# Kernel tuning notes

Measured on AMD Instinct MI355X. Metric: run time of the kernel, lower is better.

## Reference

```python
import jax, jax.numpy as jnp
import numpy as np

V, N = 3, 32768
C2, C3 = 256, 32          # feat_ch_2D, feat_ch_3D
H = W = 128               # 2D feature map size
D = 32                    # 3D volume feature size
CIN = C2 + C3             # 288, MLP in_channels


def setup_inputs() -> dict:
    key = jax.random.key(0)
    ks = jax.random.split(key, 16)
    sc = 0.02
    inp = {
        'pts': jax.random.uniform(ks[0], (1, N, 3), minval=-0.5, maxval=0.5),
        'pts_proj': jax.random.uniform(ks[1], (1, N, 2), minval=-1.0, maxval=1.0),
        'img_feat0': jax.random.normal(ks[2], (V, C2, H, W)),
        'img_feat1': jax.random.normal(ks[3], (V, C2, H, W)),
        'vol_feat0': jax.random.normal(ks[4], (V, C3, D, D, D)),
        'vol_feat1': jax.random.normal(ks[5], (V, C3, D, D, D)),
        'W0': jax.random.normal(ks[6], (1024, CIN)) * sc,  'b0': jnp.zeros((1024,)),
        'W1': jax.random.normal(ks[7], (512, CIN + 1024)) * sc, 'b1': jnp.zeros((512,)),
        'W2': jax.random.normal(ks[8], (256, CIN + 512)) * sc,  'b2': jnp.zeros((256,)),
        'W3': jax.random.normal(ks[9], (128, CIN + 256)) * sc,  'b3': jnp.zeros((128,)),
        'W4': jax.random.normal(ks[10], (1, 128)) * sc,         'b4': jnp.zeros((1,)),
        'mean_num': 3,
    }
    return inp


def _gs2d(feat, gx, gy):
    # feat: [C,H,W]; gx,gy: [N] normalized coords in [-1,1]
    C, Hh, Ww = feat.shape
    ix = jnp.clip(((gx + 1.0) * Ww - 1.0) * 0.5, 0.0, Ww - 1.0)  # align_corners=False, border pad
    iy = jnp.clip(((gy + 1.0) * Hh - 1.0) * 0.5, 0.0, Hh - 1.0)
    x0f, y0f = jnp.floor(ix), jnp.floor(iy)
    wx, wy = ix - x0f, iy - y0f
    x0 = x0f.astype(jnp.int32); x1 = jnp.minimum(x0 + 1, Ww - 1)
    y0 = y0f.astype(jnp.int32); y1 = jnp.minimum(y0 + 1, Hh - 1)
    v00 = feat[:, y0, x0]; v01 = feat[:, y0, x1]
    v10 = feat[:, y1, x0]; v11 = feat[:, y1, x1]
    return (v00 * (1 - wy) * (1 - wx) + v01 * (1 - wy) * wx
            + v10 * wy * (1 - wx) + v11 * wy * wx)  # [C,N]


def _gs3d(feat, gx, gy, gz):
    # feat: [C,D,H,W]; grid x->W, y->H, z->D (torch grid_sample convention)
    C, Dd, Hh, Ww = feat.shape
    ix = jnp.clip(((gx + 1.0) * Ww - 1.0) * 0.5, 0.0, Ww - 1.0)
    iy = jnp.clip(((gy + 1.0) * Hh - 1.0) * 0.5, 0.0, Hh - 1.0)
    iz = jnp.clip(((gz + 1.0) * Dd - 1.0) * 0.5, 0.0, Dd - 1.0)
    x0f, y0f, z0f = jnp.floor(ix), jnp.floor(iy), jnp.floor(iz)
    wx, wy, wz = ix - x0f, iy - y0f, iz - z0f
    x0 = x0f.astype(jnp.int32); x1 = jnp.minimum(x0 + 1, Ww - 1)
    y0 = y0f.astype(jnp.int32); y1 = jnp.minimum(y0 + 1, Hh - 1)
    z0 = z0f.astype(jnp.int32); z1 = jnp.minimum(z0 + 1, Dd - 1)
    def g(zi, yi, xi):
        return feat[:, zi, yi, xi]  # [C,N]
    out = (g(z0, y0, x0) * (1 - wz) * (1 - wy) * (1 - wx)
           + g(z0, y0, x1) * (1 - wz) * (1 - wy) * wx
           + g(z0, y1, x0) * (1 - wz) * wy * (1 - wx)
           + g(z0, y1, x1) * (1 - wz) * wy * wx
           + g(z1, y0, x0) * wz * (1 - wy) * (1 - wx)
           + g(z1, y0, x1) * wz * (1 - wy) * wx
           + g(z1, y1, x0) * wz * wy * (1 - wx)
           + g(z1, y1, x1) * wz * wy * wx)
    return out  # [C,N]


def _lrelu(x):
    return jnp.where(x >= 0, x, 0.2 * x)


def _conv1x1(Wm, bm, x):
    # x: [V,C,N] -> [V,O,N]
    return jnp.einsum('oc,vcn->von', Wm, x) + bm[None, :, None]


def _mlp0(x, W0, b0, W1, b1, W2, b2, W3, b3):
    out = _lrelu(_conv1x1(W0, b0, x))
    out = _lrelu(_conv1x1(W1, b1, jnp.concatenate([x, out], axis=1)))
    out = _lrelu(_conv1x1(W2, b2, jnp.concatenate([x, out], axis=1)))
    out = _lrelu(_conv1x1(W3, b3, jnp.concatenate([x, out], axis=1)))
    return out  # [V,128,N]


def _forward(pts, pts_proj, img_feats, vol_feats,
             W0, b0, W1, b1, W2, b2, W3, b3, W4, b4, mean_num):
    v = img_feats[0].shape[0]
    gx2 = jnp.broadcast_to(pts_proj[:, :, 0], (v, pts_proj.shape[1]))
    gy2 = jnp.broadcast_to(pts_proj[:, :, 1], (v, pts_proj.shape[1]))
    p = pts * 2.0  # pts *= 2.0 before 3D sampling
    gx3 = jnp.broadcast_to(p[:, :, 0], (v, p.shape[1]))
    gy3 = jnp.broadcast_to(p[:, :, 1], (v, p.shape[1]))
    gz3 = jnp.broadcast_to(p[:, :, 2], (v, p.shape[1]))
    outs = []
    for img_feat, vol_feat in zip(img_feats, vol_feats):
        f2 = jax.vmap(_gs2d)(img_feat, gx2, gy2)            # [V,C2,N]
        f3 = jax.vmap(_gs3d)(vol_feat, gx3, gy3, gz3)       # [V,C3,N]
        pt_feat = jnp.concatenate([f2, f3], axis=1)         # [V,288,N]
        pt_out0 = _mlp0(pt_feat, W0, b0, W1, b1, W2, b2, W3, b3)
        pt_out0_mean = jnp.mean(pt_out0[:mean_num], axis=0, keepdims=True)  # [1,128,N]
        sdf = jax.nn.sigmoid(_conv1x1(W4, b4, pt_out0_mean))                # [1,1,N]
        outs.append(jnp.transpose(sdf, (0, 2, 1)))                          # [1,N,1]
    return tuple(outs)


def reference(pts, pts_proj, img_feat0, img_feat1, vol_feat0, vol_feat1,
              W0, b0, W1, b1, W2, b2, W3, b3, W4, b4, mean_num):
    return _forward(pts, pts_proj, [img_feat0, img_feat1], [vol_feat0, vol_feat1],
                    W0, b0, W1, b1, W2, b2, W3, b3, W4, b4, mean_num)
```

## Files before the change

kernel.cpp:

```cpp
#include <hip/hip_runtime.h>
#include <hip/hip_bf16.h>

#define NV 3
#define NPTS 32768
#define C2C 256
#define C3C 32
#define CINC 288
#define CINP 320
#define HH 128
#define WWW 128
#define DDD 32

typedef short bh8 __attribute__((ext_vector_type(8)));
typedef float fx4 __attribute__((ext_vector_type(4)));
typedef unsigned short us4 __attribute__((ext_vector_type(4)));

__device__ __forceinline__ float b2f(unsigned short u) {
    unsigned int x = ((unsigned int)u) << 16;
    return __uint_as_float(x);
}
__device__ __forceinline__ unsigned short f2b(float f) {
    unsigned int x = __float_as_uint(f);
    unsigned int r = (x + 0x7FFFu + ((x >> 16) & 1u)) >> 16;
    return (unsigned short)r;
}

__device__ __forceinline__ void gl2lds16(const unsigned short* g, unsigned short* l) {
    __builtin_amdgcn_global_load_lds(
        (const __attribute__((address_space(1))) unsigned int*)g,
        (__attribute__((address_space(3))) unsigned int*)l, 16, 0, 0);
}

__device__ __forceinline__ int xcd_swz(int orig, int nwg) {
    int xcd = orig & 7;
    int q = nwg >> 3, r = nwg & 7;
    int base = (xcd < r) ? xcd * (q + 1) : r * (q + 1) + (xcd - r) * q;
    return base + (orig >> 3);
}

__global__ void k_wpad4(const float* __restrict__ s0, const float* __restrict__ s1,
                        const float* __restrict__ s2, const float* __restrict__ s3,
                        unsigned short* __restrict__ d0, unsigned short* __restrict__ d1,
                        unsigned short* __restrict__ d2, unsigned short* __restrict__ d3) {
    const int Ms[4] = {1024, 512, 256, 128};
    const int Kps[4] = {320, 1344, 832, 576};
    int i = blockIdx.y;
    int M = Ms[i], Kp = Kps[i];
    int idx = blockIdx.x * 256 + threadIdx.x;
    if (idx >= M * Kp) return;
    const float* src = (i == 0) ? s0 : (i == 1) ? s1 : (i == 2) ? s2 : s3;
    unsigned short* dst = (i == 0) ? d0 : (i == 1) ? d1 : (i == 2) ? d2 : d3;
    int m = idx / Kp, k = idx - m * Kp;
    int Ksrc = Kp - 32;
    float v;
    if (k < CINC) v = src[(size_t)m * Ksrc + k];
    else if (k < CINP) v = 0.0f;
    else v = src[(size_t)m * Ksrc + (k - 32)];
    dst[idx] = f2b(v);
}

__global__ void k_timg(const float* __restrict__ in0, const float* __restrict__ in1,
                       unsigned short* __restrict__ out, size_t lvlStride) {
    int lvl = blockIdx.z >> 2, cb = blockIdx.z & 3;
    const float* in = lvl ? in1 : in0;
    int v = blockIdx.x >> 7, y = blockIdx.x & 127;
    int x0 = blockIdx.y << 6, c0 = cb << 6;
    __shared__ float t[64][65];
    int tx = threadIdx.x & 63, tg = threadIdx.x >> 6;
    const float* src = in + (((size_t)(v * C2C + c0) * HH + y) * WWW + x0);
#pragma unroll
    for (int i = 0; i < 16; i++) {
        int cl = tg * 16 + i;
        t[cl][tx] = src[(size_t)cl * (HH * WWW) + tx];
    }
    __syncthreads();
    unsigned short* dst = out + lvl * lvlStride + ((size_t)(v * HH + y) * WWW + x0) * C2C + c0;
#pragma unroll
    for (int i = 0; i < 16; i++) {
        int xl = tg * 16 + i;
        dst[(size_t)xl * C2C + tx] = f2b(t[tx][xl]);
    }
}

__global__ void k_tvol(const float* __restrict__ in0, const float* __restrict__ in1,
                       unsigned short* __restrict__ out, size_t lvlStride) {
    int lvl = blockIdx.z;
    const float* in = lvl ? in1 : in0;
    int v = blockIdx.x;
    int s0 = blockIdx.y << 8;
    __shared__ float t[32][257];
    int tid = threadIdx.x;
    const float* src = in + (size_t)v * C3C * 32768 + s0;
#pragma unroll
    for (int c = 0; c < 32; c++) t[c][tid] = src[(size_t)c * 32768 + tid];
    __syncthreads();
    unsigned short* dst = out + lvl * lvlStride + ((size_t)v * 32768 + s0) * C3C;
    int c = tid & 31, sb = tid >> 5;
#pragma unroll
    for (int j = 0; j < 32; j++) {
        int sl = j * 8 + sb;
        dst[(size_t)sl * C3C + c] = f2b(t[c][sl]);
    }
}

__device__ __forceinline__ void sample_body(const float* __restrict__ pts, const float* __restrict__ proj,
                         const unsigned short* __restrict__ imgT, const unsigned short* __restrict__ volT,
                         unsigned short* __restrict__ ptT, int n0, int Nk) {
    int w = threadIdx.x >> 6, l = threadIdx.x & 63;
    int i = blockIdx.x * 4 + w;
    int v = blockIdx.y;
    int n = n0 + i;
    unsigned short* dstRow = ptT + (size_t)(v * Nk + i) * CINP;

    {
        float gx = proj[n * 2 + 0], gy = proj[n * 2 + 1];
        float ix = fminf(fmaxf(((gx + 1.0f) * (float)WWW - 1.0f) * 0.5f, 0.0f), (float)(WWW - 1));
        float iy = fminf(fmaxf(((gy + 1.0f) * (float)HH - 1.0f) * 0.5f, 0.0f), (float)(HH - 1));
        float x0f = floorf(ix), y0f = floorf(iy);
        float wx = ix - x0f, wy = iy - y0f;
        int x0 = (int)x0f, y0 = (int)y0f;
        int x1 = min(x0 + 1, WWW - 1), y1 = min(y0 + 1, HH - 1);
        const unsigned short* base = imgT + (size_t)v * HH * WWW * C2C;
        us4 a = *((const us4*)(base + ((size_t)(y0 * WWW + x0)) * C2C) + l);
        us4 b = *((const us4*)(base + ((size_t)(y0 * WWW + x1)) * C2C) + l);
        us4 c = *((const us4*)(base + ((size_t)(y1 * WWW + x0)) * C2C) + l);
        us4 d = *((const us4*)(base + ((size_t)(y1 * WWW + x1)) * C2C) + l);
        float w00 = (1.0f - wy) * (1.0f - wx), w01 = (1.0f - wy) * wx;
        float w10 = wy * (1.0f - wx), w11 = wy * wx;
        us4 rv;
#pragma unroll
        for (int r = 0; r < 4; r++) {
            float f = b2f(a[r]) * w00 + b2f(b[r]) * w01 + b2f(c[r]) * w10 + b2f(d[r]) * w11;
            rv[r] = f2b(f);
        }
        *(us4*)(dstRow + l * 4) = rv;
    }
    {
        float gx = pts[n * 3 + 0] * 2.0f, gy = pts[n * 3 + 1] * 2.0f, gz = pts[n * 3 + 2] * 2.0f;
        float ix = fminf(fmaxf(((gx + 1.0f) * (float)DDD - 1.0f) * 0.5f, 0.0f), (float)(DDD - 1));
        float iy = fminf(fmaxf(((gy + 1.0f) * (float)DDD - 1.0f) * 0.5f, 0.0f), (float)(DDD - 1));
        float iz = fminf(fmaxf(((gz + 1.0f) * (float)DDD - 1.0f) * 0.5f, 0.0f), (float)(DDD - 1));
        float x0f = floorf(ix), y0f = floorf(iy), z0f = floorf(iz);
        float wx = ix - x0f, wy = iy - y0f, wz = iz - z0f;
        int x0 = (int)x0f, y0 = (int)y0f, z0 = (int)z0f;
        int x1 = min(x0 + 1, DDD - 1), y1 = min(y0 + 1, DDD - 1), z1 = min(z0 + 1, DDD - 1);
        int c = l & 31, zs = l >> 5;
        int zi = zs ? z1 : z0;
        float wzs = zs ? wz : (1.0f - wz);
        const unsigned short* base = volT + (size_t)v * 32768 * C3C;
        float f00 = b2f(base[((size_t)((zi * 32 + y0) * 32 + x0)) * C3C + c]);
        float f01 = b2f(base[((size_t)((zi * 32 + y0) * 32 + x1)) * C3C + c]);
        float f10 = b2f(base[((size_t)((zi * 32 + y1) * 32 + x0)) * C3C + c]);
        float f11 = b2f(base[((size_t)((zi * 32 + y1) * 32 + x1)) * C3C + c]);
        float r = (f00 * (1.0f - wy) * (1.0f - wx) + f01 * (1.0f - wy) * wx +
                   f10 * wy * (1.0f - wx) + f11 * wy * wx) * wzs;
        float other = __shfl_xor(r, 32);
        r += other;
        if (zs == 0) dstRow[C2C + c] = f2b(r);
    }
    if (l < 8) *(us4*)(dstRow + CINC + l * 4) = (us4){0, 0, 0, 0};
}

__global__ __launch_bounds__(256) void k_sampleL0(const float* p, const float* pr, const unsigned short* im,
                                                  const unsigned short* vo, unsigned short* pt, int n0, int Nk) {
    sample_body(p, pr, im, vo, pt, n0, Nk);
}
__global__ __launch_bounds__(256) void k_sampleL1(const float* p, const float* pr, const unsigned short* im,
                                                  const unsigned short* vo, unsigned short* pt, int n0, int Nk) {
    sample_body(p, pr, im, vo, pt, n0, Nk);
}

template <int K2, int M>
__device__ __forceinline__ void gemm128_body(const unsigned short* __restrict__ A,
                                             const unsigned short* __restrict__ B1,
                                             const unsigned short* __restrict__ B2,
                                             const float* __restrict__ bias,
                                             unsigned short* __restrict__ C) {
    constexpr int K1 = CINP;
    constexpr int K = K1 + K2;
    constexpr int nt1 = K1 / 32;
    constexpr int nt = K / 32;
    __shared__ unsigned short Ash[3][128 * 32];
    __shared__ unsigned short Bsh[3][128 * 32];
    int tid = threadIdx.x;
    int w = tid >> 6, l = tid & 63;
    int la = l & 15, lg = l >> 4;
    int wm = w & 1, wn = w >> 1;
    int gx = gridDim.x;
    int nwg = gx * gridDim.y;
    int bid = xcd_swz(blockIdx.y * gx + blockIdx.x, nwg);
    int mBlk = (bid % gx) * 128;
    int nBlk = (bid / gx) * 128;
    int sRow = l >> 2, sCol = (l & 3) * 8;
    int r0 = w * 32 + sRow, r1 = r0 + 16;

    const unsigned short* Ag = A + (size_t)mBlk * K;
    const unsigned short* B1g = B1 + (size_t)nBlk * K1;
    const unsigned short* B2g = (K2 > 0) ? (B2 + (size_t)nBlk * K2) : (const unsigned short*)0;

    fx4 acc[4][4];
#pragma unroll
    for (int mi = 0; mi < 4; mi++)
#pragma unroll
        for (int ni = 0; ni < 4; ni++) acc[mi][ni] = (fx4){0.f, 0.f, 0.f, 0.f};

    auto stage = [&](int t, int b) {
        const unsigned short* as = Ag + t * 32 + sCol;
        gl2lds16(as + (size_t)r0 * K, &Ash[b][r0 * 32 + sCol]);
        gl2lds16(as + (size_t)r1 * K, &Ash[b][r1 * 32 + sCol]);
        const unsigned short* bs;
        size_t ldb;
        if (t < nt1) { bs = B1g + t * 32 + sCol; ldb = (size_t)K1; }
        else         { bs = B2g + (t - nt1) * 32 + sCol; ldb = (size_t)K2; }
        gl2lds16(bs + (size_t)r0 * ldb, &Bsh[b][r0 * 32 + sCol]);
        gl2lds16(bs + (size_t)r1 * ldb, &Bsh[b][r1 * 32 + sCol]);
    };

    stage(0, 0);
    if (nt > 1) stage(1, 1);
    asm volatile("s_waitcnt vmcnt(4)" ::: "memory");
    __builtin_amdgcn_s_barrier();
    int cur = 0, nxt2 = 2;
    for (int t = 0; t < nt; t++) {
        if (t + 2 < nt) stage(t + 2, nxt2);
        bh8 af[4], bfv[4];
#pragma unroll
        for (int mi = 0; mi < 4; mi++) af[mi] = *(const bh8*)&Ash[cur][(wm * 64 + mi * 16 + la) * 32 + lg * 8];
#pragma unroll
        for (int ni = 0; ni < 4; ni++) bfv[ni] = *(const bh8*)&Bsh[cur][(wn * 64 + ni * 16 + la) * 32 + lg * 8];
#pragma unroll
        for (int mi = 0; mi < 4; mi++)
#pragma unroll
            for (int ni = 0; ni < 4; ni++)
                acc[mi][ni] = __builtin_amdgcn_mfma_f32_16x16x32_bf16(af[mi], bfv[ni], acc[mi][ni], 0, 0, 0);
        asm volatile("s_waitcnt lgkmcnt(0)" ::: "memory");
        if (t + 2 < nt)      asm volatile("s_waitcnt vmcnt(4)" ::: "memory");
        else if (t + 1 < nt) asm volatile("s_waitcnt vmcnt(0)" ::: "memory");
        __builtin_amdgcn_s_barrier();
        cur = (cur == 2) ? 0 : cur + 1;
        nxt2 = (nxt2 == 2) ? 0 : nxt2 + 1;
    }

#pragma unroll
    for (int mi = 0; mi < 4; mi++) {
        int m0 = mBlk + wm * 64 + mi * 16 + lg * 4;
        fx4 bb = *(const fx4*)(bias + m0);
#pragma unroll
        for (int ni = 0; ni < 4; ni++) {
            int n = nBlk + wn * 64 + ni * 16 + la;
            us4 rv;
#pragma unroll
            for (int r = 0; r < 4; r++) {
                float x = acc[mi][ni][r] + bb[r];
                x = (x >= 0.0f) ? x : 0.2f * x;
                rv[r] = f2b(x);
            }
            *(us4*)(C + (size_t)n * M + m0) = rv;
        }
    }
}

__global__ __launch_bounds__(256) void k_g0L0(const unsigned short* A, const unsigned short* B1,
                                              const float* b, unsigned short* C) { gemm128_body<0, 1024>(A, B1, nullptr, b, C); }
__global__ __launch_bounds__(256) void k_g0L1(const unsigned short* A, const unsigned short* B1,
                                              const float* b, unsigned short* C) { gemm128_body<0, 1024>(A, B1, nullptr, b, C); }
__global__ __launch_bounds__(256) void k_g2L0(const unsigned short* A, const unsigned short* B1, const unsigned short* B2,
                                              const float* b, unsigned short* C) { gemm128_body<512, 256>(A, B1, B2, b, C); }
__global__ __launch_bounds__(256) void k_g2L1(const unsigned short* A, const unsigned short* B1, const unsigned short* B2,
                                              const float* b, unsigned short* C) { gemm128_body<512, 256>(A, B1, B2, b, C); }
__global__ __launch_bounds__(256) void k_g3L0(const unsigned short* A, const unsigned short* B1, const unsigned short* B2,
                                              const float* b, unsigned short* C) { gemm128_body<256, 128>(A, B1, B2, b, C); }
__global__ __launch_bounds__(256) void k_g3L1(const unsigned short* A, const unsigned short* B1, const unsigned short* B2,
                                              const float* b, unsigned short* C) { gemm128_body<256, 128>(A, B1, B2, b, C); }

__device__ __forceinline__ void g1_body(const unsigned short* __restrict__ A,
                                        const unsigned short* __restrict__ B1,
                                        const unsigned short* __restrict__ B2,
                                        const float* __restrict__ bias,
                                        unsigned short* __restrict__ C) {
    constexpr int Kp = 1344;
    constexpr int K2 = 1024;
    constexpr int M = 512;
    constexpr int nt = Kp >> 6;
    __shared__ unsigned short As[2][256 * 64];
    __shared__ unsigned short Bs[2][256 * 64];
    int tid = threadIdx.x;
    int w = tid >> 6, l = tid & 63;
    int la = l & 15, lg = l >> 4;
    int wm = w >> 2, wn = w & 3;
    int gx = gridDim.x;
    int nwg = gx * gridDim.y;
    int bid = xcd_swz(blockIdx.y * gx + blockIdx.x, nwg);
    int mBlk = (bid % gx) * 256;
    int nBlk = (bid / gx) * 256;

    const unsigned short* Ag = A + (size_t)mBlk * Kp;

    fx4 acc[8][4];
#pragma unroll
    for (int mi = 0; mi < 8; mi++)
#pragma unroll
        for (int ni = 0; ni < 4; ni++) acc[mi][ni] = (fx4){0.f, 0.f, 0.f, 0.f};

    auto stageB = [&](int t, int nxt) {
        const unsigned short* bsrc;
        size_t ldb;
        int kc;
        if (t < 5) { bsrc = B1; ldb = CINP; kc = t * 64; }
        else       { bsrc = B2; ldb = (size_t)K2; kc = (t - 5) * 64; }
        bsrc += (size_t)nBlk * ldb + kc;
#pragma unroll
        for (int h = 0; h < 2; h++)
#pragma unroll
            for (int j = 0; j < 2; j++) {
                int idx = j * 512 + tid;
                int r = (h << 7) + (idx >> 3);
                int c = (idx & 7) ^ (r & 7);
                gl2lds16(bsrc + (size_t)r * ldb + c * 8, &Bs[nxt][(h << 13) + idx * 8]);
            }
    };
    auto stageA1 = [&](int t, int nxt) {
        const unsigned short* asrc = Ag + t * 64;
#pragma unroll
        for (int h = 0; h < 2; h++) {
            int idx = tid;
            int r = (h << 7) + (idx >> 3);
            int c = (idx & 7) ^ (r & 7);
            gl2lds16(asrc + (size_t)r * Kp + c * 8, &As[nxt][(h << 13) + idx * 8]);
        }
    };
    auto stageA2 = [&](int t, int nxt) {
        const unsigned short* asrc = Ag + t * 64;
#pragma unroll
        for (int h = 0; h < 2; h++) {
            int idx = 512 + tid;
            int r = (h << 7) + (idx >> 3);
            int c = (idx & 7) ^ (r & 7);
            gl2lds16(asrc + (size_t)r * Kp + c * 8, &As[nxt][(h << 13) + idx * 8]);
        }
    };

    stageB(0, 0);
    stageA1(0, 0);
    stageA2(0, 0);
    asm volatile("s_waitcnt vmcnt(0)" ::: "memory");
    __builtin_amdgcn_s_barrier();

    for (int t = 0; t < nt; t++) {
        int cur = t & 1;
        const unsigned short* Ab = &As[cur][0];
        const unsigned short* Bb = &Bs[cur][0];
        bh8 afr[4][2];
#pragma unroll
        for (int p = 0; p < 4; p++) {
            int qm = p >> 1, qn = p & 1;
            if (qn == 0) {
#pragma unroll
                for (int m2 = 0; m2 < 4; m2++)
#pragma unroll
                    for (int s = 0; s < 2; s++) {
                        int row = wm * 128 + (qm * 4 + m2) * 16 + la;
                        int c = (s * 4 + lg) ^ (row & 7);
                        afr[m2][s] = *(const bh8*)&Ab[row * 64 + c * 8];
                    }
            }
            bh8 bfr[2][2];
#pragma unroll
            for (int n2 = 0; n2 < 2; n2++)
#pragma unroll
                for (int s = 0; s < 2; s++) {
                    int row = wn * 64 + (qn * 2 + n2) * 16 + la;
                    int c = (s * 4 + lg) ^ (row & 7);
                    bfr[n2][s] = *(const bh8*)&Bb[row * 64 + c * 8];
                }
            if (p == 0 && t + 1 < nt) stageB(t + 1, cur ^ 1);
            if (p == 1 && t + 1 < nt) stageA1(t + 1, cur ^ 1);
            if (p == 2 && t + 1 < nt) stageA2(t + 1, cur ^ 1);
            __builtin_amdgcn_s_barrier();
            __builtin_amdgcn_s_setprio(1);
#pragma unroll
            for (int m2 = 0; m2 < 4; m2++)
#pragma unroll
                for (int n2 = 0; n2 < 2; n2++)
#pragma unroll
                    for (int s = 0; s < 2; s++)
                        acc[qm * 4 + m2][qn * 2 + n2] = __builtin_amdgcn_mfma_f32_16x16x32_bf16(
                            afr[m2][s], bfr[n2][s], acc[qm * 4 + m2][qn * 2 + n2], 0, 0, 0);
            __builtin_amdgcn_s_setprio(0);
            if (p == 1) {
                if (t + 1 < nt) asm volatile("s_waitcnt vmcnt(6)" ::: "memory");
                else            asm volatile("s_waitcnt vmcnt(0)" ::: "memory");
            }
            if (p == 3) {
                asm volatile("s_waitcnt lgkmcnt(0)" ::: "memory");
                if (t + 1 < nt) asm volatile("s_waitcnt vmcnt(2)" ::: "memory");
            }
            __builtin_amdgcn_s_barrier();
        }
    }

#pragma unroll
    for (int mi = 0; mi < 8; mi++) {
        int m0 = mBlk + wm * 128 + mi * 16 + lg * 4;
        fx4 bb = *(const fx4*)(bias + m0);
#pragma unroll
        for (int ni = 0; ni < 4; ni++) {
            int n = nBlk + wn * 64 + ni * 16 + la;
            us4 rv;
#pragma unroll
            for (int r = 0; r < 4; r++) {
                float x = acc[mi][ni][r] + bb[r];
                x = (x >= 0.0f) ? x : 0.2f * x;
                rv[r] = f2b(x);
            }
            *(us4*)(C + (size_t)n * M + m0) = rv;
        }
    }
}

__global__ __launch_bounds__(512) void k_g1L0(const unsigned short* A, const unsigned short* B1, const unsigned short* B2,
                                              const float* b, unsigned short* C) { g1_body(A, B1, B2, b, C); }
__global__ __launch_bounds__(512) void k_g1L1(const unsigned short* A, const unsigned short* B1, const unsigned short* B2,
                                              const float* b, unsigned short* C) { g1_body(A, B1, B2, b, C); }

__device__ __forceinline__ void head_body(const unsigned short* __restrict__ o3, const float* __restrict__ W4,
                       const float* __restrict__ b4, const int* __restrict__ mn_p,
                       float* __restrict__ out, int n0, int Nk, int level) {
    int wv = threadIdx.x >> 6, l = threadIdx.x & 63;
    int sub = l >> 4, cl = l & 15;
    int i = blockIdx.x * 16 + wv * 4 + sub;
    if (i >= Nk) return;
    int mn = *mn_p;
    if (mn > NV) mn = NV;
    if (mn < 1) mn = 1;
    fx4 w0 = *(const fx4*)(W4 + cl * 8);
    fx4 w1 = *(const fx4*)(W4 + cl * 8 + 4);
    float s = 0.0f;
    for (int v = 0; v < mn; v++) {
        bh8 x = *(const bh8*)(o3 + (size_t)(v * Nk + i) * 128 + cl * 8);
#pragma unroll
        for (int r = 0; r < 4; r++) s += w0[r] * b2f((unsigned short)x[r]);
#pragma unroll
        for (int r = 0; r < 4; r++) s += w1[r] * b2f((unsigned short)x[4 + r]);
    }
#pragma unroll
    for (int m = 1; m < 16; m <<= 1) s += __shfl_xor(s, m);
    if (cl == 0) {
        s = s / (float)mn + b4[0];
        out[(size_t)level * NPTS + n0 + i] = 1.0f / (1.0f + expf(-s));
    }
}

__global__ __launch_bounds__(256) void k_headL0(const unsigned short* o3, const float* W4, const float* b4,
                                                const int* mn, float* out, int n0, int Nk) {
    head_body(o3, W4, b4, mn, out, n0, Nk, 0);
}
__global__ __launch_bounds__(256) void k_headL1(const unsigned short* o3, const float* W4, const float* b4,
                                                const int* mn, float* out, int n0, int Nk) {
    head_body(o3, W4, b4, mn, out, n0, Nk, 1);
}

extern "C" void kernel_launch(void* const* d_in, const int* in_sizes, int n_in,
                              void* d_out, int out_size, void* d_ws, size_t ws_size,
                              hipStream_t stream) {
    const float* pts = (const float*)d_in[0];
    const float* proj = (const float*)d_in[1];
    const float* img[2] = {(const float*)d_in[2], (const float*)d_in[3]};
    const float* vol[2] = {(const float*)d_in[4], (const float*)d_in[5]};
    const float* Wf[4] = {(const float*)d_in[6], (const float*)d_in[8], (const float*)d_in[10], (const float*)d_in[12]};
    const float* bf[4] = {(const float*)d_in[7], (const float*)d_in[9], (const float*)d_in[11], (const float*)d_in[13]};
    const float* W4 = (const float*)d_in[14];
    const float* b4 = (const float*)d_in[15];
    const int* mn = (const int*)d_in[16];
    float* out = (float*)d_out;

    const int Kp[4] = {320, 1344, 832, 576};
    const int Msz[4] = {1024, 512, 256, 128};

    char* ws = (char*)d_ws;
    size_t off = 0;
    auto alloc = [&](size_t bytes) -> char* {
        char* p = ws + off;
        off = (off + bytes + 255) & ~(size_t)255;
        return p;
    };

    const size_t imgStride = (size_t)NV * HH * WWW * C2C;
    const size_t volStride = (size_t)NV * 32768 * C3C;

    unsigned short* Wb[4];
    for (int i = 0; i < 4; i++) Wb[i] = (unsigned short*)alloc((size_t)Msz[i] * Kp[i] * 2);
    unsigned short* imgT = (unsigned short*)alloc(2 * imgStride * 2);
    unsigned short* volT = (unsigned short*)alloc(2 * volStride * 2);
    size_t fixed = off;

    const size_t perPt = (size_t)NV * 2 * (CINP + 1024 + 512);
    int Nk = NPTS;
    if (fixed + (size_t)Nk * perPt + 4096 > ws_size) {
        size_t avail = (ws_size > fixed + 4096) ? (ws_size - fixed - 4096) : 0;
        long nk = (long)(avail / perPt);
        nk = (nk / 512) * 512;
        if (nk < 512) nk = 512;
        if (nk > NPTS) nk = NPTS;
        Nk = (int)nk;
    }
    unsigned short* ptT = (unsigned short*)alloc((size_t)NV * Nk * CINP * 2);
    unsigned short* o0 = (unsigned short*)alloc((size_t)NV * Nk * 1024 * 2);
    unsigned short* o1 = (unsigned short*)alloc((size_t)NV * Nk * 512 * 2);
    unsigned short* o2 = o0;
    unsigned short* o3 = o0 + (size_t)NV * Nk * 256;

    k_wpad4<<<dim3(2688, 4), 256, 0, stream>>>(Wf[0], Wf[1], Wf[2], Wf[3], Wb[0], Wb[1], Wb[2], Wb[3]);
    k_timg<<<dim3(NV * HH, WWW / 64, 8), 256, 0, stream>>>(img[0], img[1], imgT, imgStride);
    k_tvol<<<dim3(NV, 32768 / 256, 2), 256, 0, stream>>>(vol[0], vol[1], volT, volStride);

    for (int n0 = 0; n0 < NPTS; n0 += Nk) {
        int nk = NPTS - n0 < Nk ? NPTS - n0 : Nk;
        int NC = NV * nk;
        k_sampleL0<<<dim3(nk / 4, NV), 256, 0, stream>>>(pts, proj, imgT, volT, ptT, n0, nk);
        k_g0L0<<<dim3(1024 / 128, NC / 128), 256, 0, stream>>>(Wb[0], ptT, bf[0], o0);
        k_g1L0<<<dim3(512 / 256, NC / 256), 512, 0, stream>>>(Wb[1], ptT, o0, bf[1], o1);
        k_g2L0<<<dim3(256 / 128, NC / 128), 256, 0, stream>>>(Wb[2], ptT, o1, bf[2], o2);
        k_g3L0<<<dim3(128 / 128, NC / 128), 256, 0, stream>>>(Wb[3], ptT, o2, bf[3], o3);
        k_headL0<<<(nk + 15) / 16, 256, 0, stream>>>(o3, W4, b4, mn, out, n0, nk);
        k_sampleL1<<<dim3(nk / 4, NV), 256, 0, stream>>>(pts, proj, imgT + imgStride, volT + volStride, ptT, n0, nk);
        k_g0L1<<<dim3(1024 / 128, NC / 128), 256, 0, stream>>>(Wb[0], ptT, bf[0], o0);
        k_g1L1<<<dim3(512 / 256, NC / 256), 512, 0, stream>>>(Wb[1], ptT, o0, bf[1], o1);
        k_g2L1<<<dim3(256 / 128, NC / 128), 256, 0, stream>>>(Wb[2], ptT, o1, bf[2], o2);
        k_g3L1<<<dim3(128 / 128, NC / 128), 256, 0, stream>>>(Wb[3], ptT, o2, bf[3], o3);
        k_headL1<<<(nk + 15) / 16, 256, 0, stream>>>(o3, W4, b4, mn, out, n0, nk);
    }
}
```

Before: 1.059 ms.

## Use 256x256 tile GEMM for layer 0 and merge prep kernels into one launch

The first MLP layer GEMM now runs through the 256x256, 512-thread templated kernel previously used only for layer 1, in place of the 128x128 kernel. This raises per-block data reuse and cuts the number of blocks. The three preprocessing kernels (weight padding/cast, image transpose, volume transpose) are merged into one launch that dispatches on block index, removing two launches. The risk is that layer 0 has a short K (320), so the large tile gives few pipeline iterations and fewer blocks for occupancy.

New measurement: 1.065 ms. About the same (+0.6%).

```diff
diff --git a/kernel.cpp b/kernel.cpp
--- a/kernel.cpp
+++ b/kernel.cpp
@@ -38,68 +38,74 @@
     return base + (orig >> 3);
 }
 
-__global__ void k_wpad4(const float* __restrict__ s0, const float* __restrict__ s1,
-                        const float* __restrict__ s2, const float* __restrict__ s3,
-                        unsigned short* __restrict__ d0, unsigned short* __restrict__ d1,
-                        unsigned short* __restrict__ d2, unsigned short* __restrict__ d3) {
-    const int Ms[4] = {1024, 512, 256, 128};
-    const int Kps[4] = {320, 1344, 832, 576};
-    int i = blockIdx.y;
-    int M = Ms[i], Kp = Kps[i];
-    int idx = blockIdx.x * 256 + threadIdx.x;
-    if (idx >= M * Kp) return;
-    const float* src = (i == 0) ? s0 : (i == 1) ? s1 : (i == 2) ? s2 : s3;
-    unsigned short* dst = (i == 0) ? d0 : (i == 1) ? d1 : (i == 2) ? d2 : d3;
-    int m = idx / Kp, k = idx - m * Kp;
-    int Ksrc = Kp - 32;
-    float v;
-    if (k < CINC) v = src[(size_t)m * Ksrc + k];
-    else if (k < CINP) v = 0.0f;
-    else v = src[(size_t)m * Ksrc + (k - 32)];
-    dst[idx] = f2b(v);
-}
-
-__global__ void k_timg(const float* __restrict__ in0, const float* __restrict__ in1,
-                       unsigned short* __restrict__ out, size_t lvlStride) {
-    int lvl = blockIdx.z >> 2, cb = blockIdx.z & 3;
-    const float* in = lvl ? in1 : in0;
-    int v = blockIdx.x >> 7, y = blockIdx.x & 127;
-    int x0 = blockIdx.y << 6, c0 = cb << 6;
-    __shared__ float t[64][65];
-    int tx = threadIdx.x & 63, tg = threadIdx.x >> 6;
-    const float* src = in + (((size_t)(v * C2C + c0) * HH + y) * WWW + x0);
-#pragma unroll
-    for (int i = 0; i < 16; i++) {
-        int cl = tg * 16 + i;
-        t[cl][tx] = src[(size_t)cl * (HH * WWW) + tx];
-    }
-    __syncthreads();
-    unsigned short* dst = out + lvl * lvlStride + ((size_t)(v * HH + y) * WWW + x0) * C2C + c0;
-#pragma unroll
-    for (int i = 0; i < 16; i++) {
-        int xl = tg * 16 + i;
-        dst[(size_t)xl * C2C + tx] = f2b(t[tx][xl]);
-    }
-}
-
-__global__ void k_tvol(const float* __restrict__ in0, const float* __restrict__ in1,
-                       unsigned short* __restrict__ out, size_t lvlStride) {
-    int lvl = blockIdx.z;
-    const float* in = lvl ? in1 : in0;
-    int v = blockIdx.x;
-    int s0 = blockIdx.y << 8;
-    __shared__ float t[32][257];
-    int tid = threadIdx.x;
-    const float* src = in + (size_t)v * C3C * 32768 + s0;
-#pragma unroll
-    for (int c = 0; c < 32; c++) t[c][tid] = src[(size_t)c * 32768 + tid];
-    __syncthreads();
-    unsigned short* dst = out + lvl * lvlStride + ((size_t)v * 32768 + s0) * C3C;
-    int c = tid & 31, sb = tid >> 5;
-#pragma unroll
-    for (int j = 0; j < 32; j++) {
-        int sl = j * 8 + sb;
-        dst[(size_t)sl * C3C + c] = f2b(t[c][sl]);
+__global__ __launch_bounds__(256) void k_prep(
+    const float* __restrict__ s0, const float* __restrict__ s1,
+    const float* __restrict__ s2, const float* __restrict__ s3,
+    unsigned short* __restrict__ d0, unsigned short* __restrict__ d1,
+    unsigned short* __restrict__ d2, unsigned short* __restrict__ d3,
+    const float* __restrict__ img0, const float* __restrict__ img1,
+    unsigned short* __restrict__ imgT, size_t imgStride,
+    const float* __restrict__ vol0, const float* __restrict__ vol1,
+    unsigned short* __restrict__ volT, size_t volStride) {
+    __shared__ float smem[32 * 257];
+    int b = blockIdx.x;
+    if (b < 5088) {
+        int base, M, Kp;
+        const float* src;
+        unsigned short* dst;
+        if (b < 1280)      { base = 0;    M = 1024; Kp = 320;  src = s0; dst = d0; }
+        else if (b < 3968) { base = 1280; M = 512;  Kp = 1344; src = s1; dst = d1; }
+        else if (b < 4800) { base = 3968; M = 256;  Kp = 832;  src = s2; dst = d2; }
+        else               { base = 4800; M = 128;  Kp = 576;  src = s3; dst = d3; }
+        int idx = (b - base) * 256 + threadIdx.x;
+        if (idx >= M * Kp) return;
+        int m = idx / Kp, k = idx - m * Kp;
+        int Ksrc = Kp - 32;
+        float v;
+        if (k < CINC) v = src[(size_t)m * Ksrc + k];
+        else if (k < CINP) v = 0.0f;
+        else v = src[(size_t)m * Ksrc + (k - 32)];
+        dst[idx] = f2b(v);
+    } else if (b < 11232) {
+        int id = b - 5088;
+        int bx = id % 384, by = (id / 384) & 1, bz = id / 768;
+        int lvl = bz >> 2, cb = bz & 3;
+        const float* in = lvl ? img1 : img0;
+        int v = bx >> 7, y = bx & 127;
+        int x0 = by << 6, c0 = cb << 6;
+        float (*t)[65] = (float(*)[65])smem;
+        int tx = threadIdx.x & 63, tg = threadIdx.x >> 6;
+        const float* src = in + (((size_t)(v * C2C + c0) * HH + y) * WWW + x0);
+#pragma unroll
+        for (int i = 0; i < 16; i++) {
+            int cl = tg * 16 + i;
+            t[cl][tx] = src[(size_t)cl * (HH * WWW) + tx];
+        }
+        __syncthreads();
+        unsigned short* dst = imgT + lvl * imgStride + ((size_t)(v * HH + y) * WWW + x0) * C2C + c0;
+#pragma unroll
+        for (int i = 0; i < 16; i++) {
+            int xl = tg * 16 + i;
+            dst[(size_t)xl * C2C + tx] = f2b(t[tx][xl]);
+        }
+    } else {
+        int id = b - 11232;
+        int v = id % 3, sy = (id / 3) & 127, lvl = id / 384;
+        const float* in = lvl ? vol1 : vol0;
+        int s0i = sy << 8;
+        float (*t)[257] = (float(*)[257])smem;
+        int tid = threadIdx.x;
+        const float* src = in + (size_t)v * C3C * 32768 + s0i;
+#pragma unroll
+        for (int c = 0; c < 32; c++) t[c][tid] = src[(size_t)c * 32768 + tid];
+        __syncthreads();
+        unsigned short* dst = volT + lvl * volStride + ((size_t)v * 32768 + s0i) * C3C;
+        int c = tid & 31, sb = tid >> 5;
+#pragma unroll
+        for (int j = 0; j < 32; j++) {
+            int sl = j * 8 + sb;
+            dst[(size_t)sl * C3C + c] = f2b(t[c][sl]);
+        }
     }
 }
 
@@ -260,10 +266,6 @@
     }
 }
 
-__global__ __launch_bounds__(256) void k_g0L0(const unsigned short* A, const unsigned short* B1,
-                                              const float* b, unsigned short* C) { gemm128_body<0, 1024>(A, B1, nullptr, b, C); }
-__global__ __launch_bounds__(256) void k_g0L1(const unsigned short* A, const unsigned short* B1,
-                                              const float* b, unsigned short* C) { gemm128_body<0, 1024>(A, B1, nullptr, b, C); }
 __global__ __launch_bounds__(256) void k_g2L0(const unsigned short* A, const unsigned short* B1, const unsigned short* B2,
                                               const float* b, unsigned short* C) { gemm128_body<512, 256>(A, B1, B2, b, C); }
 __global__ __launch_bounds__(256) void k_g2L1(const unsigned short* A, const unsigned short* B1, const unsigned short* B2,
@@ -273,15 +275,13 @@
 __global__ __launch_bounds__(256) void k_g3L1(const unsigned short* A, const unsigned short* B1, const unsigned short* B2,
                                               const float* b, unsigned short* C) { gemm128_body<256, 128>(A, B1, B2, b, C); }
 
-__device__ __forceinline__ void g1_body(const unsigned short* __restrict__ A,
-                                        const unsigned short* __restrict__ B1,
-                                        const unsigned short* __restrict__ B2,
-                                        const float* __restrict__ bias,
-                                        unsigned short* __restrict__ C) {
-    constexpr int Kp = 1344;
-    constexpr int K2 = 1024;
-    constexpr int M = 512;
-    constexpr int nt = Kp >> 6;
+template <int KP, int K2, int M>
+__device__ __forceinline__ void g1t_body(const unsigned short* __restrict__ A,
+                                         const unsigned short* __restrict__ B1,
+                                         const unsigned short* __restrict__ B2,
+                                         const float* __restrict__ bias,
+                                         unsigned short* __restrict__ C) {
+    constexpr int nt = KP >> 6;
     __shared__ unsigned short As[2][256 * 64];
     __shared__ unsigned short Bs[2][256 * 64];
     int tid = threadIdx.x;
@@ -294,7 +294,7 @@
     int mBlk = (bid % gx) * 256;
     int nBlk = (bid / gx) * 256;
 
-    const unsigned short* Ag = A + (size_t)mBlk * Kp;
+    const unsigned short* Ag = A + (size_t)mBlk * KP;
 
     fx4 acc[8][4];
 #pragma unroll
@@ -326,7 +326,7 @@
             int idx = tid;
             int r = (h << 7) + (idx >> 3);
             int c = (idx & 7) ^ (r & 7);
-            gl2lds16(asrc + (size_t)r * Kp + c * 8, &As[nxt][(h << 13) + idx * 8]);
+            gl2lds16(asrc + (size_t)r * KP + c * 8, &As[nxt][(h << 13) + idx * 8]);
         }
     };
     auto stageA2 = [&](int t, int nxt) {
@@ -336,7 +336,7 @@
             int idx = 512 + tid;
             int r = (h << 7) + (idx >> 3);
             int c = (idx & 7) ^ (r & 7);
-            gl2lds16(asrc + (size_t)r * Kp + c * 8, &As[nxt][(h << 13) + idx * 8]);
+            gl2lds16(asrc + (size_t)r * KP + c * 8, &As[nxt][(h << 13) + idx * 8]);
         }
     };
 
@@ -418,10 +418,14 @@
     }
 }
 
+__global__ __launch_bounds__(512) void k_g0L0(const unsigned short* A, const unsigned short* B1,
+                                              const float* b, unsigned short* C) { g1t_body<320, 0, 1024>(A, B1, nullptr, b, C); }
+__global__ __launch_bounds__(512) void k_g0L1(const unsigned short* A, const unsigned short* B1,
+                                              const float* b, unsigned short* C) { g1t_body<320, 0, 1024>(A, B1, nullptr, b, C); }
 __global__ __launch_bounds__(512) void k_g1L0(const unsigned short* A, const unsigned short* B1, const unsigned short* B2,
-                                              const float* b, unsigned short* C) { g1_body(A, B1, B2, b, C); }
+                                              const float* b, unsigned short* C) { g1t_body<1344, 1024, 512>(A, B1, B2, b, C); }
 __global__ __launch_bounds__(512) void k_g1L1(const unsigned short* A, const unsigned short* B1, const unsigned short* B2,
-                                              const float* b, unsigned short* C) { g1_body(A, B1, B2, b, C); }
+                                              const float* b, unsigned short* C) { g1t_body<1344, 1024, 512>(A, B1, B2, b, C); }
 
 __device__ __forceinline__ void head_body(const unsigned short* __restrict__ o3, const float* __restrict__ W4,
                        const float* __restrict__ b4, const int* __restrict__ mn_p,
@@ -510,21 +514,20 @@
     unsigned short* o2 = o0;
     unsigned short* o3 = o0 + (size_t)NV * Nk * 256;
 
-    k_wpad4<<<dim3(2688, 4), 256, 0, stream>>>(Wf[0], Wf[1], Wf[2], Wf[3], Wb[0], Wb[1], Wb[2], Wb[3]);
-    k_timg<<<dim3(NV * HH, WWW / 64, 8), 256, 0, stream>>>(img[0], img[1], imgT, imgStride);
-    k_tvol<<<dim3(NV, 32768 / 256, 2), 256, 0, stream>>>(vol[0], vol[1], volT, volStride);
+    k_prep<<<12000, 256, 0, stream>>>(Wf[0], Wf[1], Wf[2], Wf[3], Wb[0], Wb[1], Wb[2], Wb[3],
+                                      img[0], img[1], imgT, imgStride, vol[0], vol[1], volT, volStride);
 
     for (int n0 = 0; n0 < NPTS; n0 += Nk) {
         int nk = NPTS - n0 < Nk ? NPTS - n0 : Nk;
         int NC = NV * nk;
         k_sampleL0<<<dim3(nk / 4, NV), 256, 0, stream>>>(pts, proj, imgT, volT, ptT, n0, nk);
-        k_g0L0<<<dim3(1024 / 128, NC / 128), 256, 0, stream>>>(Wb[0], ptT, bf[0], o0);
+        k_g0L0<<<dim3(1024 / 256, NC / 256), 512, 0, stream>>>(Wb[0], ptT, bf[0], o0);
         k_g1L0<<<dim3(512 / 256, NC / 256), 512, 0, stream>>>(Wb[1], ptT, o0, bf[1], o1);
         k_g2L0<<<dim3(256 / 128, NC / 128), 256, 0, stream>>>(Wb[2], ptT, o1, bf[2], o2);
         k_g3L0<<<dim3(128 / 128, NC / 128), 256, 0, stream>>>(Wb[3], ptT, o2, bf[3], o3);
         k_headL0<<<(nk + 15) / 16, 256, 0, stream>>>(o3, W4, b4, mn, out, n0, nk);
         k_sampleL1<<<dim3(nk / 4, NV), 256, 0, stream>>>(pts, proj, imgT + imgStride, volT + volStride, ptT, n0, nk);
-        k_g0L1<<<dim3(1024 / 128, NC / 128), 256, 0, stream>>>(Wb[0], ptT, bf[0], o0);
+        k_g0L1<<<dim3(1024 / 256, NC / 256), 512, 0, stream>>>(Wb[0], ptT, bf[0], o0);
         k_g1L1<<<dim3(512 / 256, NC / 256), 512, 0, stream>>>(Wb[1], ptT, o0, bf[1], o1);
         k_g2L1<<<dim3(256 / 128, NC / 128), 256, 0, stream>>>(Wb[2], ptT, o1, bf[2], o2);
         k_g3L1<<<dim3(128 / 128, NC / 128), 256, 0, stream>>>(Wb[3], ptT, o2, bf[3], o3);
```
